# Kernel optimization log

Hardware: AMD Instinct MI355X
Metric: run time of the kernel (lower is better)

The kernel has to match this reference:

```python
import jax, jax.numpy as jnp
import numpy as np

B, S, D, H, DK, DFF = 4, 1024, 1024, 16, 64, 4096
EPS = 1e-5


def layer_norm(x, g, b):
    m = jnp.mean(x, axis=-1, keepdims=True)
    v = jnp.var(x, axis=-1, keepdims=True)
    return (x - m) * jax.lax.rsqrt(v + EPS) * g + b


def setup_inputs() -> dict:
    key = jax.random.key(0)
    ks = jax.random.split(key, 12)
    sc = 0.02
    return {
        "x":    jax.random.normal(ks[0], (B, S, D), jnp.float32),
        # per-head Q/K/V projections, stacked over heads: [H, D, DK]
        "Wq":   jax.random.normal(ks[1], (H, D, DK), jnp.float32) * sc,
        "bq":   jnp.zeros((H, DK), jnp.float32),
        "Wk":   jax.random.normal(ks[2], (H, D, DK), jnp.float32) * sc,
        "bk":   jnp.zeros((H, DK), jnp.float32),
        "Wv":   jax.random.normal(ks[3], (H, D, DK), jnp.float32) * sc,
        "bv":   jnp.zeros((H, DK), jnp.float32),
        # output projection: [H*DK, D]
        "Wo":   jax.random.normal(ks[4], (H * DK, D), jnp.float32) * sc,
        "bo":   jnp.zeros((D,), jnp.float32),
        # FFN
        "W1":   jax.random.normal(ks[5], (D, DFF), jnp.float32) * sc,
        "b1":   jnp.zeros((DFF,), jnp.float32),
        "W2":   jax.random.normal(ks[6], (DFF, D), jnp.float32) * sc,
        "b2":   jnp.zeros((D,), jnp.float32),
        # LayerNorms
        "g1":   jnp.ones((D,), jnp.float32),
        "be1":  jnp.zeros((D,), jnp.float32),
        "g2":   jnp.ones((D,), jnp.float32),
        "be2":  jnp.zeros((D,), jnp.float32),
    }


def reference(x, Wq, bq, Wk, bk, Wv, bv, Wo, bo, W1, b1, W2, b2, g1, be1, g2, be2):
    # batched multi-head attention (original loops per head; math identical)
    q = jnp.einsum("bsd,hdk->bhsk", x, Wq) + bq[None, :, None, :]
    k = jnp.einsum("bsd,hdk->bhsk", x, Wk) + bk[None, :, None, :]
    v = jnp.einsum("bsd,hdk->bhsk", x, Wv) + bv[None, :, None, :]
    scale = 1.0 / jnp.sqrt(jnp.asarray(DK, x.dtype))
    scores = jnp.einsum("bhsk,bhtk->bhst", q * scale, k)
    attn = jax.nn.softmax(scores, axis=-1)  # dropout = eval-mode identity
    o = jnp.einsum("bhst,bhtk->bhsk", attn, v)
    # torch.cat over heads along dim 2 -> [B, S, H*DK]
    o = jnp.transpose(o, (0, 2, 1, 3)).reshape(B, S, H * DK)
    att = o @ Wo + bo
    # post-attn: residual of LayerNorm(att)
    x = x + layer_norm(att, g1, be1)
    # FFN
    pos = jax.nn.relu(x @ W1 + b1) @ W2 + b2
    x = x + layer_norm(pos, g2, be2)
    return x
```

## Files before the change

### kernel.cpp

```cpp
#include <hip/hip_runtime.h>
#include <hip/hip_bf16.h>

typedef unsigned short u16;
typedef short bf16x8_t __attribute__((ext_vector_type(8)));
typedef float f32x4_t  __attribute__((ext_vector_type(4)));

__device__ __forceinline__ u16 f2bf(float f) {
    __hip_bfloat16 h = __float2bfloat16(f);
    union { __hip_bfloat16 b; u16 u; } cv; cv.b = h; return cv.u;
}

__device__ __forceinline__ void g2l16(const void* g, void* l) {
    __builtin_amdgcn_global_load_lds(
        (const __attribute__((address_space(1))) unsigned int*)g,
        (__attribute__((address_space(3))) unsigned int*)l, 16, 0, 0);
}

__global__ __launch_bounds__(256) void k_cast_bf16v(const float* __restrict__ in,
                                                    u16* __restrict__ out, int n4) {
    int i = blockIdx.x * 256 + threadIdx.x;
    if (i < n4) {
        float4 f = ((const float4*)in)[i];
        ushort4 o;
        o.x = f2bf(f.x); o.y = f2bf(f.y); o.z = f2bf(f.z); o.w = f2bf(f.w);
        ((ushort4*)out)[i] = o;
    }
}

__global__ __launch_bounds__(256)
void k_transpose3(const float* __restrict__ Wo, const float* __restrict__ W1,
                  const float* __restrict__ W2, u16* __restrict__ Wot,
                  u16* __restrict__ W1t, u16* __restrict__ W2t) {
    int id = blockIdx.x;
    const float* in; u16* out; int R, C, tx, ty;
    if (id < 256)       { in = Wo; out = Wot; R = 1024; C = 1024; tx = id & 15; ty = id >> 4; }
    else if (id < 1280) { id -= 256; in = W1; out = W1t; R = 1024; C = 4096; tx = id & 63; ty = id >> 6; }
    else                { id -= 1280; in = W2; out = W2t; R = 4096; C = 1024; tx = id & 15; ty = id >> 4; }
    __shared__ float t[64][65];
    int r0 = ty * 64, c0 = tx * 64;
    int lc = threadIdx.x & 63, lr = threadIdx.x >> 6;
#pragma unroll
    for (int p = 0; p < 16; ++p) {
        int rr = p * 4 + lr;
        t[rr][lc] = in[(size_t)(r0 + rr) * C + c0 + lc];
    }
    __syncthreads();
#pragma unroll
    for (int p = 0; p < 16; ++p) {
        int cc = p * 4 + lr;
        out[(size_t)(c0 + cc) * R + r0 + lc] = f2bf(t[lc][cc]);
    }
}

__global__ __launch_bounds__(256)
void k_qkvw_t(const float* __restrict__ Wq, const float* __restrict__ Wk,
              const float* __restrict__ Wv, u16* __restrict__ out) {
    const float* in = blockIdx.z == 0 ? Wq : (blockIdx.z == 1 ? Wk : Wv);
    in += (size_t)blockIdx.y * 65536;
    u16* o = out + ((size_t)blockIdx.z * 1024 + blockIdx.y * 64) * 1024;
    __shared__ float t[64][65];
    int d0 = blockIdx.x * 64;
    int lc = threadIdx.x & 63, lr = threadIdx.x >> 6;
#pragma unroll
    for (int p = 0; p < 16; ++p) {
        int rr = p * 4 + lr;
        t[rr][lc] = in[(size_t)(d0 + rr) * 64 + lc];
    }
    __syncthreads();
#pragma unroll
    for (int p = 0; p < 16; ++p) {
        int cc = p * 4 + lr;
        o[(size_t)cc * 1024 + d0 + lc] = f2bf(t[lc][cc]);
    }
}

__global__ __launch_bounds__(256)
void k_vt(const u16* __restrict__ V, u16* __restrict__ VT) {
    __shared__ u16 t[64 * 72];
    int bh = blockIdx.y, s0 = blockIdx.x * 64;
    const u16* Vp = V + (size_t)bh * 65536;
    u16* Tp = VT + (size_t)bh * 65536;
    int tid = threadIdx.x;
    int r = tid >> 3, c = (tid & 7) * 8;
    *(uint4*)&t[r * 72 + c]        = *(const uint4*)&Vp[(size_t)(s0 + r) * 64 + c];
    *(uint4*)&t[(r + 32) * 72 + c] = *(const uint4*)&Vp[(size_t)(s0 + r + 32) * 64 + c];
    __syncthreads();
    int d = tid >> 2, sl0 = (tid & 3) * 16;
    uint4 outv[2];
    u16* ov = (u16*)outv;
#pragma unroll
    for (int j = 0; j < 16; ++j) ov[j] = t[(sl0 + j) * 72 + d];
    *(uint4*)&Tp[(size_t)d * 1024 + s0 + sl0]     = outv[0];
    *(uint4*)&Tp[(size_t)d * 1024 + s0 + sl0 + 8] = outv[1];
}

template<int EPI>
__global__ __launch_bounds__(256)
void k_gemm_bt(const u16* __restrict__ A, const u16* __restrict__ Bt,
               const float* __restrict__ bias0, const float* __restrict__ bias1,
               const float* __restrict__ bias2, void* __restrict__ out,
               int M, int N, int K, int kchunk)
{
    __shared__ __align__(16) u16 As[2 * 128 * 32];
    __shared__ __align__(16) u16 Bs[2 * 128 * 32];
    int tid = threadIdx.x;
    int wave = tid >> 6, lane = tid & 63;
    int row0 = blockIdx.y * 128, col0 = blockIdx.x * 128;
    int z = blockIdx.z;
    int kbeg = z * kchunk;

    int lrow = lane >> 2, lcol = (lane & 3) * 8;
    const u16* pA0 = A  + (size_t)(row0 + wave * 16 + lrow) * K + kbeg + lcol;
    const u16* pA1 = pA0 + (size_t)64 * K;
    const u16* pB0 = Bt + (size_t)(col0 + wave * 16 + lrow) * K + kbeg + lcol;
    const u16* pB1 = pB0 + (size_t)64 * K;
    u16* lA0 = &As[wave * 512];
    u16* lA1 = &As[2048 + wave * 512];
    u16* lB0 = &Bs[wave * 512];
    u16* lB1 = &Bs[2048 + wave * 512];

    int wm = (wave >> 1) * 64, wn = (wave & 1) * 64;
    int quad = lane >> 4, l16 = lane & 15;

    f32x4_t acc[4][4];
#pragma unroll
    for (int i = 0; i < 4; i++)
#pragma unroll
        for (int j = 0; j < 4; j++) acc[i][j] = f32x4_t{0.f, 0.f, 0.f, 0.f};

    for (int kk = 0; kk < kchunk; kk += 64) {
        __syncthreads();
        g2l16(pA0, lA0);      g2l16(pA1, lA1);
        g2l16(pA0 + 32, lA0 + 4096); g2l16(pA1 + 32, lA1 + 4096);
        g2l16(pB0, lB0);      g2l16(pB1, lB1);
        g2l16(pB0 + 32, lB0 + 4096); g2l16(pB1 + 32, lB1 + 4096);
        pA0 += 64; pA1 += 64; pB0 += 64; pB1 += 64;
        __syncthreads();

#pragma unroll
        for (int s = 0; s < 2; ++s) {
            const u16* as = &As[s * 4096];
            const u16* bs = &Bs[s * 4096];
            bf16x8_t a[4], b[4];
#pragma unroll
            for (int i = 0; i < 4; ++i)
                a[i] = *(const bf16x8_t*)&as[(wm + i * 16 + l16) * 32 + quad * 8];
#pragma unroll
            for (int j = 0; j < 4; ++j)
                b[j] = *(const bf16x8_t*)&bs[(wn + j * 16 + l16) * 32 + quad * 8];
#pragma unroll
            for (int i = 0; i < 4; ++i)
#pragma unroll
                for (int j = 0; j < 4; ++j)
                    acc[i][j] = __builtin_amdgcn_mfma_f32_16x16x32_bf16(a[i], b[j], acc[i][j], 0, 0, 0);
        }
    }

#pragma unroll
    for (int i = 0; i < 4; ++i)
#pragma unroll
        for (int j = 0; j < 4; ++j)
#pragma unroll
            for (int r = 0; r < 4; ++r) {
                int row = row0 + wm + i * 16 + quad * 4 + r;
                int col = col0 + wn + j * 16 + l16;
                float v = acc[i][j][r];
                if (EPI == 0) {
                    ((float*)out)[(size_t)z * M * N + (size_t)row * N + col] = v;
                } else if (EPI == 1) {
                    ((u16*)out)[(size_t)row * N + col] = f2bf(fmaxf(v + bias0[col], 0.f));
                } else {
                    int proj = col >> 10, within = col & 1023;
                    const float* bp = proj == 0 ? bias0 : (proj == 1 ? bias1 : bias2);
                    v += bp[within];
                    if (proj == 0) v *= 0.18033688f;
                    int h = within >> 6, kq = within & 63;
                    int b_ = row >> 10, s_ = row & 1023;
                    size_t bh = (size_t)((b_ << 4) + h);
                    ((u16*)out)[(size_t)proj * 4194304 + bh * 65536 + (s_ << 6) + kq] = f2bf(v);
                }
            }
}

__global__ __launch_bounds__(512, 4)
void k_attn(const u16* __restrict__ Qg, const u16* __restrict__ Kg,
            const u16* __restrict__ VTg, u16* __restrict__ Og)
{
    __shared__ __align__(16) u16 Ks[64 * 64];
    __shared__ __align__(16) u16 Vs[64 * 64];
    __shared__ __align__(16) u16 Ps[128 * 64];

    int tid = threadIdx.x, wave = tid >> 6, lane = tid & 63;
    int quad = lane >> 4, l16 = lane & 15;
    int bh = blockIdx.y;
    int q0 = blockIdx.x * 128;
    int wrow = wave * 16;

    const u16* Qp  = Qg  + (size_t)bh * 65536;
    const u16* Kp  = Kg  + (size_t)bh * 65536;
    const u16* VTp = VTg + (size_t)bh * 65536;

    int arow_g = q0 + wrow + l16;
    bf16x8_t aq0 = *(const bf16x8_t*)&Qp[(size_t)arow_g * 64 + quad * 8];
    bf16x8_t aq1 = *(const bf16x8_t*)&Qp[(size_t)arow_g * 64 + 32 + quad * 8];

    int srow = tid >> 3, scb = tid & 7;
    uint4 kreg = *(const uint4*)&Kp[(size_t)srow * 64 + scb * 8];
    uint4 vreg = *(const uint4*)&VTp[(size_t)srow * 1024 + scb * 8];
    u16* kdst = &Ks[srow * 64 + ((scb ^ (srow & 7)) * 8)];
    u16* vdst = &Vs[srow * 64 + ((scb ^ (srow & 7)) * 8)];

    f32x4_t o[4], lsum;
#pragma unroll
    for (int nt = 0; nt < 4; ++nt) o[nt] = f32x4_t{0.f, 0.f, 0.f, 0.f};
    lsum = f32x4_t{0.f, 0.f, 0.f, 0.f};

    bf16x8_t ones;
#pragma unroll
    for (int j = 0; j < 8; ++j) ones[j] = (short)0x3F80;

    int a7 = l16 & 7;

    for (int kv0 = 0; kv0 < 1024; kv0 += 64) {
        __syncthreads();
        *(uint4*)kdst = kreg;
        *(uint4*)vdst = vreg;
        __syncthreads();
        if (kv0 < 960) {
            kreg = *(const uint4*)&Kp[(size_t)(kv0 + 64 + srow) * 64 + scb * 8];
            vreg = *(const uint4*)&VTp[(size_t)srow * 1024 + kv0 + 64 + scb * 8];
        }

        f32x4_t s[4];
#pragma unroll
        for (int nt = 0; nt < 4; ++nt) {
            int brow = nt * 16 + l16;
            bf16x8_t bk0 = *(const bf16x8_t*)&Ks[brow * 64 + ((quad ^ a7) * 8)];
            bf16x8_t bk1 = *(const bf16x8_t*)&Ks[brow * 64 + (((4 + quad) ^ a7) * 8)];
            s[nt] = __builtin_amdgcn_mfma_f32_16x16x32_bf16(aq0, bk0, f32x4_t{0.f,0.f,0.f,0.f}, 0, 0, 0);
            s[nt] = __builtin_amdgcn_mfma_f32_16x16x32_bf16(aq1, bk1, s[nt], 0, 0, 0);
        }

#pragma unroll
        for (int nt = 0; nt < 4; ++nt) {
            int pcb = nt * 2 + (l16 >> 3);
#pragma unroll
            for (int r = 0; r < 4; ++r) {
                float p = exp2f(s[nt][r]);
                int pr = wrow + quad * 4 + r;
                Ps[pr * 64 + ((pcb ^ (pr & 7)) * 8) + (l16 & 7)] = f2bf(p);
            }
        }

        int arow = wrow + l16;
        bf16x8_t ap0 = *(const bf16x8_t*)&Ps[arow * 64 + ((quad ^ a7) * 8)];
        bf16x8_t ap1 = *(const bf16x8_t*)&Ps[arow * 64 + (((4 + quad) ^ a7) * 8)];
#pragma unroll
        for (int nt = 0; nt < 4; ++nt) {
            int vrow = nt * 16 + l16;
            bf16x8_t bv0 = *(const bf16x8_t*)&Vs[vrow * 64 + ((quad ^ a7) * 8)];
            bf16x8_t bv1 = *(const bf16x8_t*)&Vs[vrow * 64 + (((4 + quad) ^ a7) * 8)];
            o[nt] = __builtin_amdgcn_mfma_f32_16x16x32_bf16(ap0, bv0, o[nt], 0, 0, 0);
            o[nt] = __builtin_amdgcn_mfma_f32_16x16x32_bf16(ap1, bv1, o[nt], 0, 0, 0);
        }
        lsum = __builtin_amdgcn_mfma_f32_16x16x32_bf16(ap0, ones, lsum, 0, 0, 0);
        lsum = __builtin_amdgcn_mfma_f32_16x16x32_bf16(ap1, ones, lsum, 0, 0, 0);
    }

    int b = bh >> 4, h = bh & 15;
    float invl[4];
#pragma unroll
    for (int r = 0; r < 4; ++r) invl[r] = 1.f / lsum[r];
#pragma unroll
    for (int nt = 0; nt < 4; ++nt)
#pragma unroll
        for (int r = 0; r < 4; ++r) {
            int srow2 = q0 + wrow + quad * 4 + r;
            Og[(size_t)(b * 1024 + srow2) * 1024 + (h << 6) + nt * 16 + l16] = f2bf(o[nt][r] * invl[r]);
        }
}

__global__ __launch_bounds__(256)
void k_ln2(const float* __restrict__ p0, const float* __restrict__ p1,
           const float* __restrict__ bias, const float* __restrict__ resid,
           const float* __restrict__ g, const float* __restrict__ be,
           float* __restrict__ out, u16* __restrict__ outb)
{
    int row = blockIdx.x, tid = threadIdx.x;
    size_t base = (size_t)row * 1024;
    float xv[4]; float s = 0.f, sq = 0.f;
#pragma unroll
    for (int i = 0; i < 4; i++) {
        int c = tid + i * 256;
        xv[i] = p0[base + c] + p1[base + c] + bias[c];
        s += xv[i]; sq += xv[i] * xv[i];
    }
#pragma unroll
    for (int off = 32; off; off >>= 1) { s += __shfl_down(s, off); sq += __shfl_down(sq, off); }
    __shared__ float ss[4], ssq[4];
    int wv = tid >> 6;
    if ((tid & 63) == 0) { ss[wv] = s; ssq[wv] = sq; }
    __syncthreads();
    s  = ss[0] + ss[1] + ss[2] + ss[3];
    sq = ssq[0] + ssq[1] + ssq[2] + ssq[3];
    float mean = s * (1.f / 1024.f);
    float var  = sq * (1.f / 1024.f) - mean * mean;
    float rstd = rsqrtf(var + 1e-5f);
#pragma unroll
    for (int i = 0; i < 4; i++) {
        int c = tid + i * 256;
        float y = resid[base + c] + (xv[i] - mean) * rstd * g[c] + be[c];
        out[base + c] = y;
        if (outb) outb[base + c] = f2bf(y);
    }
}

extern "C" void kernel_launch(void* const* d_in, const int* in_sizes, int n_in,
                              void* d_out, int out_size, void* d_ws, size_t ws_size,
                              hipStream_t stream) {
    const float* x   = (const float*)d_in[0];
    const float* Wq  = (const float*)d_in[1];
    const float* bq  = (const float*)d_in[2];
    const float* Wk  = (const float*)d_in[3];
    const float* bk  = (const float*)d_in[4];
    const float* Wv  = (const float*)d_in[5];
    const float* bv  = (const float*)d_in[6];
    const float* Wo  = (const float*)d_in[7];
    const float* bo  = (const float*)d_in[8];
    const float* W1  = (const float*)d_in[9];
    const float* b1  = (const float*)d_in[10];
    const float* W2  = (const float*)d_in[11];
    const float* b2  = (const float*)d_in[12];
    const float* g1  = (const float*)d_in[13];
    const float* be1 = (const float*)d_in[14];
    const float* g2  = (const float*)d_in[15];
    const float* be2 = (const float*)d_in[16];
    float* out = (float*)d_out;

    char* w = (char*)d_ws;
    u16*   Xb    = (u16*)(w);
    u16*   VTb   = (u16*)(w);
    u16*   Wqkvt = (u16*)(w + 8388608);
    u16*   Wot   = (u16*)(w + 14680064);
    u16*   W1t   = (u16*)(w + 16777216);
    u16*   W2t   = (u16*)(w + 25165824);
    u16*   Qb    = (u16*)(w + 33554432);
    u16*   Kb    = (u16*)(w + 41943040);
    u16*   Vb    = (u16*)(w + 50331648);
    u16*   Oc    = (u16*)(w + 58720256);
    float* part  = (float*)(w + 67108864);
    float* x1    = (float*)(w + 100663296);
    u16*   x1b   = (u16*)(w + 117440512);
    u16*   hb    = (u16*)(w + 125829120);

    k_cast_bf16v<<<4096, 256, 0, stream>>>(x, Xb, 1048576);
    k_qkvw_t<<<dim3(16, 16, 3), 256, 0, stream>>>(Wq, Wk, Wv, Wqkvt);
    k_transpose3<<<2304, 256, 0, stream>>>(Wo, W1, W2, Wot, W1t, W2t);

    k_gemm_bt<2><<<dim3(24, 32), 256, 0, stream>>>(Xb, Wqkvt, bq, bk, bv, Qb, 4096, 3072, 1024, 1024);

    k_vt<<<dim3(16, 64), 256, 0, stream>>>(Vb, VTb);

    k_attn<<<dim3(8, 64), 512, 0, stream>>>(Qb, Kb, VTb, Oc);

    k_gemm_bt<0><<<dim3(8, 32, 2), 256, 0, stream>>>(Oc, Wot, nullptr, nullptr, nullptr, part, 4096, 1024, 1024, 512);

    k_ln2<<<4096, 256, 0, stream>>>(part, part + 4194304, bo, x, g1, be1, x1, x1b);

    k_gemm_bt<1><<<dim3(32, 32), 256, 0, stream>>>(x1b, W1t, b1, nullptr, nullptr, hb, 4096, 4096, 1024, 1024);

    k_gemm_bt<0><<<dim3(8, 32, 2), 256, 0, stream>>>(hb, W2t, nullptr, nullptr, nullptr, part, 4096, 1024, 4096, 2048);

    k_ln2<<<4096, 256, 0, stream>>>(part, part + 4194304, b2, x1, g2, be2, out, nullptr);
}
```

Measured before the change: 366.2 us.

## Use 256x128 tiles with 512 threads for QKV and FFN1 GEMMs; drop fp32 x1

Adds a GEMM kernel with 8 waves and 256x128 output tiles that stages 64 of K per sync, and uses it for the QKV projection and the first FFN GEMM. The aim is more operand reuse per block and fewer barriers in the K loop. The second LayerNorm now reads the bf16 copy of the intermediate residual instead of an fp32 copy, which removes one fp32 write and read. The cost is lower residual precision and a larger LDS footprint per block, which may reduce occupancy.

```diff
diff --git a/kernel.cpp b/kernel.cpp
--- a/kernel.cpp
+++ b/kernel.cpp
@@ -97,8 +97,7 @@
 template<int EPI>
 __global__ __launch_bounds__(256)
 void k_gemm_bt(const u16* __restrict__ A, const u16* __restrict__ Bt,
-               const float* __restrict__ bias0, const float* __restrict__ bias1,
-               const float* __restrict__ bias2, void* __restrict__ out,
+               const float* __restrict__ bias0, void* __restrict__ out,
                int M, int N, int K, int kchunk)
 {
     __shared__ __align__(16) u16 As[2 * 128 * 32];
@@ -164,10 +163,77 @@
             for (int r = 0; r < 4; ++r) {
                 int row = row0 + wm + i * 16 + quad * 4 + r;
                 int col = col0 + wn + j * 16 + l16;
+                ((float*)out)[(size_t)z * M * N + (size_t)row * N + col] = acc[i][j][r];
+            }
+}
+
+template<int EPI>
+__global__ __launch_bounds__(512, 4)
+void k_gemm_bt2(const u16* __restrict__ A, const u16* __restrict__ Bt,
+                const float* __restrict__ bias0, const float* __restrict__ bias1,
+                const float* __restrict__ bias2, void* __restrict__ out,
+                int M, int N, int K)
+{
+    __shared__ __align__(16) u16 As[2 * 256 * 32];
+    __shared__ __align__(16) u16 Bs[2 * 128 * 32];
+    int tid = threadIdx.x;
+    int wave = tid >> 6, lane = tid & 63;
+    int row0 = blockIdx.y * 256, col0 = blockIdx.x * 128;
+
+    int lrow = lane >> 2, lcol = (lane & 3) * 8;
+    const u16* pA0 = A  + (size_t)(row0 + wave * 16 + lrow) * K + lcol;
+    const u16* pA1 = pA0 + (size_t)128 * K;
+    const u16* pB0 = Bt + (size_t)(col0 + wave * 16 + lrow) * K + lcol;
+    u16* lA0 = &As[wave * 512];
+    u16* lA1 = &As[4096 + wave * 512];
+    u16* lB0 = &Bs[wave * 512];
+
+    int wm = (wave >> 1) * 64, wn = (wave & 1) * 64;
+    int quad = lane >> 4, l16 = lane & 15;
+
+    f32x4_t acc[4][4];
+#pragma unroll
+    for (int i = 0; i < 4; i++)
+#pragma unroll
+        for (int j = 0; j < 4; j++) acc[i][j] = f32x4_t{0.f, 0.f, 0.f, 0.f};
+
+    for (int kk = 0; kk < K; kk += 64) {
+        __syncthreads();
+        g2l16(pA0, lA0);           g2l16(pA1, lA1);
+        g2l16(pA0 + 32, lA0 + 8192); g2l16(pA1 + 32, lA1 + 8192);
+        g2l16(pB0, lB0);           g2l16(pB0 + 32, lB0 + 4096);
+        pA0 += 64; pA1 += 64; pB0 += 64;
+        __syncthreads();
+
+#pragma unroll
+        for (int s = 0; s < 2; ++s) {
+            const u16* as = &As[s * 8192];
+            const u16* bs = &Bs[s * 4096];
+            bf16x8_t a[4], b[4];
+#pragma unroll
+            for (int i = 0; i < 4; ++i)
+                a[i] = *(const bf16x8_t*)&as[(wm + i * 16 + l16) * 32 + quad * 8];
+#pragma unroll
+            for (int j = 0; j < 4; ++j)
+                b[j] = *(const bf16x8_t*)&bs[(wn + j * 16 + l16) * 32 + quad * 8];
+#pragma unroll
+            for (int i = 0; i < 4; ++i)
+#pragma unroll
+                for (int j = 0; j < 4; ++j)
+                    acc[i][j] = __builtin_amdgcn_mfma_f32_16x16x32_bf16(a[i], b[j], acc[i][j], 0, 0, 0);
+        }
+    }
+
+#pragma unroll
+    for (int i = 0; i < 4; ++i)
+#pragma unroll
+        for (int j = 0; j < 4; ++j)
+#pragma unroll
+            for (int r = 0; r < 4; ++r) {
+                int row = row0 + wm + i * 16 + quad * 4 + r;
+                int col = col0 + wn + j * 16 + l16;
                 float v = acc[i][j][r];
-                if (EPI == 0) {
-                    ((float*)out)[(size_t)z * M * N + (size_t)row * N + col] = v;
-                } else if (EPI == 1) {
+                if (EPI == 1) {
                     ((u16*)out)[(size_t)row * N + col] = f2bf(fmaxf(v + bias0[col], 0.f));
                 } else {
                     int proj = col >> 10, within = col & 1023;
@@ -280,11 +346,13 @@
         }
 }
 
+template<int MODE>
 __global__ __launch_bounds__(256)
 void k_ln2(const float* __restrict__ p0, const float* __restrict__ p1,
-           const float* __restrict__ bias, const float* __restrict__ resid,
-           const float* __restrict__ g, const float* __restrict__ be,
-           float* __restrict__ out, u16* __restrict__ outb)
+           const float* __restrict__ bias, const float* __restrict__ residf,
+           const u16* __restrict__ residb, const float* __restrict__ g,
+           const float* __restrict__ be, float* __restrict__ out,
+           u16* __restrict__ outb)
 {
     int row = blockIdx.x, tid = threadIdx.x;
     size_t base = (size_t)row * 1024;
@@ -309,9 +377,16 @@
 #pragma unroll
     for (int i = 0; i < 4; i++) {
         int c = tid + i * 256;
-        float y = resid[base + c] + (xv[i] - mean) * rstd * g[c] + be[c];
-        out[base + c] = y;
-        if (outb) outb[base + c] = f2bf(y);
+        float rv;
+        if (MODE == 0) rv = residf[base + c];
+        else {
+            union { u16 u[2]; unsigned int w; float f; } cv;
+            cv.w = (unsigned int)residb[base + c] << 16;
+            rv = cv.f;
+        }
+        float y = rv + (xv[i] - mean) * rstd * g[c] + be[c];
+        if (MODE == 0) outb[base + c] = f2bf(y);
+        else           out[base + c] = y;
     }
 }
 
@@ -349,7 +424,6 @@
     u16*   Vb    = (u16*)(w + 50331648);
     u16*   Oc    = (u16*)(w + 58720256);
     float* part  = (float*)(w + 67108864);
-    float* x1    = (float*)(w + 100663296);
     u16*   x1b   = (u16*)(w + 117440512);
     u16*   hb    = (u16*)(w + 125829120);
 
@@ -357,19 +431,19 @@
     k_qkvw_t<<<dim3(16, 16, 3), 256, 0, stream>>>(Wq, Wk, Wv, Wqkvt);
     k_transpose3<<<2304, 256, 0, stream>>>(Wo, W1, W2, Wot, W1t, W2t);
 
-    k_gemm_bt<2><<<dim3(24, 32), 256, 0, stream>>>(Xb, Wqkvt, bq, bk, bv, Qb, 4096, 3072, 1024, 1024);
+    k_gemm_bt2<2><<<dim3(24, 16), 512, 0, stream>>>(Xb, Wqkvt, bq, bk, bv, Qb, 4096, 3072, 1024);
 
     k_vt<<<dim3(16, 64), 256, 0, stream>>>(Vb, VTb);
 
     k_attn<<<dim3(8, 64), 512, 0, stream>>>(Qb, Kb, VTb, Oc);
 
-    k_gemm_bt<0><<<dim3(8, 32, 2), 256, 0, stream>>>(Oc, Wot, nullptr, nullptr, nullptr, part, 4096, 1024, 1024, 512);
-
-    k_ln2<<<4096, 256, 0, stream>>>(part, part + 4194304, bo, x, g1, be1, x1, x1b);
-
-    k_gemm_bt<1><<<dim3(32, 32), 256, 0, stream>>>(x1b, W1t, b1, nullptr, nullptr, hb, 4096, 4096, 1024, 1024);
-
-    k_gemm_bt<0><<<dim3(8, 32, 2), 256, 0, stream>>>(hb, W2t, nullptr, nullptr, nullptr, part, 4096, 1024, 4096, 2048);
-
-    k_ln2<<<4096, 256, 0, stream>>>(part, part + 4194304, b2, x1, g2, be2, out, nullptr);
-}
+    k_gemm_bt<0><<<dim3(8, 32, 2), 256, 0, stream>>>(Oc, Wot, nullptr, part, 4096, 1024, 1024, 512);
+
+    k_ln2<0><<<4096, 256, 0, stream>>>(part, part + 4194304, bo, x, nullptr, g1, be1, nullptr, x1b);
+
+    k_gemm_bt2<1><<<dim3(32, 16), 512, 0, stream>>>(x1b, W1t, b1, nullptr, nullptr, hb, 4096, 4096, 1024);
+
+    k_gemm_bt<0><<<dim3(8, 32, 2), 256, 0, stream>>>(hb, W2t, nullptr, part, 4096, 1024, 4096, 2048);
+
+    k_ln2<1><<<4096, 256, 0, stream>>>(part, part + 4194304, b2, nullptr, x1b, g2, be2, out, nullptr);
+}
```

New measurement: 336.7 us. 8.0% less time.
